# Optimization experiments

Hardware: AMD Instinct MI355X
Metric: run time of the kernel (lower is better)

## Reference

```python
import jax, jax.numpy as jnp
import numpy as np

D = 1024      # query_dim
H = 16        # heads
DH = 64       # dim_head
I = H * DH    # inner_dim = 1024
DC = 768      # context_dim
FF = 4 * D    # ff inner dim = 4096
EPS = 1e-5
SCALE = DH ** -0.5


def setup_inputs() -> dict:
    key = jax.random.key(0)
    ks = jax.random.split(key, 20)
    s = 0.02
    inp = {
        'x': jax.random.normal(ks[0], (2, 2048, D), jnp.float32),
        'context': jax.random.normal(ks[1], (2, 77, DC), jnp.float32),
        'ln1_g': jnp.ones((D,), jnp.float32), 'ln1_b': jnp.zeros((D,), jnp.float32),
        'ln2_g': jnp.ones((D,), jnp.float32), 'ln2_b': jnp.zeros((D,), jnp.float32),
        'ln3_g': jnp.ones((D,), jnp.float32), 'ln3_b': jnp.zeros((D,), jnp.float32),
        'Wq1': jax.random.normal(ks[2], (D, I), jnp.float32) * s,
        'Wk1': jax.random.normal(ks[3], (D, I), jnp.float32) * s,
        'Wv1': jax.random.normal(ks[4], (D, I), jnp.float32) * s,
        'Wo1': jax.random.normal(ks[5], (I, D), jnp.float32) * s,
        'bo1': jnp.zeros((D,), jnp.float32),
        'Wq2': jax.random.normal(ks[6], (D, I), jnp.float32) * s,
        'Wk2': jax.random.normal(ks[7], (DC, I), jnp.float32) * s,
        'Wv2': jax.random.normal(ks[8], (DC, I), jnp.float32) * s,
        'Wo2': jax.random.normal(ks[9], (I, D), jnp.float32) * s,
        'bo2': jnp.zeros((D,), jnp.float32),
        'Wff1': jax.random.normal(ks[10], (D, 2 * FF), jnp.float32) * s,
        'bff1': jnp.zeros((2 * FF,), jnp.float32),
        'Wff2': jax.random.normal(ks[11], (FF, D), jnp.float32) * s,
        'bff2': jnp.zeros((D,), jnp.float32),
    }
    return inp


def layer_norm(x, g, b):
    m = jnp.mean(x, axis=-1, keepdims=True)
    v = jnp.mean(jnp.square(x - m), axis=-1, keepdims=True)
    return (x - m) * jax.lax.rsqrt(v + EPS) * g + b


def cross_attention(x, ctx, Wq, Wk, Wv, Wo, bo):
    # x: [B,N,D], ctx: [B,M,Dc]
    B, N, _ = x.shape
    M = ctx.shape[1]
    q = (x @ Wq).reshape(B, N, H, DH).transpose(0, 2, 1, 3)    # [B,H,N,DH]
    k = (ctx @ Wk).reshape(B, M, H, DH).transpose(0, 2, 1, 3)  # [B,H,M,DH]
    v = (ctx @ Wv).reshape(B, M, H, DH).transpose(0, 2, 1, 3)
    sim = jnp.einsum('bhid,bhjd->bhij', q, k) * SCALE           # [B,H,N,M]
    attn = jax.nn.softmax(sim, axis=-1)
    out = jnp.einsum('bhij,bhjd->bhid', attn, v)                # [B,H,N,DH]
    out = out.transpose(0, 2, 1, 3).reshape(B, N, I)
    return out @ Wo + bo


def reference(x, context, ln1_g, ln1_b, ln2_g, ln2_b, ln3_g, ln3_b,
              Wq1, Wk1, Wv1, Wo1, bo1, Wq2, Wk2, Wv2, Wo2, bo2,
              Wff1, bff1, Wff2, bff2):
    # self-attention
    x = cross_attention(layer_norm(x, ln1_g, ln1_b), layer_norm(x, ln1_g, ln1_b),
                        Wq1, Wk1, Wv1, Wo1, bo1) + x
    # cross-attention
    x = cross_attention(layer_norm(x, ln2_g, ln2_b), context,
                        Wq2, Wk2, Wv2, Wo2, bo2) + x
    # GEGLU feed-forward
    hg = layer_norm(x, ln3_g, ln3_b) @ Wff1 + bff1
    h, gate = hg[..., :FF], hg[..., FF:]
    ff = (h * jax.nn.gelu(gate, approximate=False)) @ Wff2 + bff2
    return ff + x
```

## Files before the change

### kernel.cpp

```cpp
#include <hip/hip_runtime.h>
#include <hip/hip_bf16.h>
#include <math.h>

typedef short short8 __attribute__((ext_vector_type(8)));
typedef float floatx4 __attribute__((ext_vector_type(4)));
typedef unsigned short u16;

#define D_MODEL 1024
#define NH 16
#define DH 64
#define FF_DIM 4096

__device__ __forceinline__ u16 f2b(float f) {
  union { float f; unsigned u; } v; v.f = f;
  unsigned r = (v.u + 0x7fffu + ((v.u >> 16) & 1u)) >> 16;
  return (u16)r;
}
__device__ __forceinline__ u16 f2b_fast(float f) {
  union { float f; unsigned u; } v; v.f = f;
  return (u16)((v.u + 0x8000u) >> 16);
}
__device__ __forceinline__ float b2f(u16 h) {
  union { unsigned u; float f; } v; v.u = ((unsigned)h) << 16;
  return v.f;
}

__device__ __forceinline__ void gl_lds16(const u16* g, u16* l) {
  __builtin_amdgcn_global_load_lds(
      (const __attribute__((address_space(1))) unsigned int*)g,
      (__attribute__((address_space(3))) unsigned int*)l, 16, 0, 0);
}

__launch_bounds__(256)
__global__ void transpose_to_bf16(const float* __restrict__ in, u16* __restrict__ out,
                                  int K, int N, float scale) {
  __shared__ float tile[32][33];
  const int n0 = blockIdx.x * 32;
  const int k0 = blockIdx.y * 32;
  const int tx = threadIdx.x & 31;
  const int ty = threadIdx.x >> 5;
#pragma unroll
  for (int i = 0; i < 4; i++) {
    int k = k0 + ty + i * 8;
    tile[ty + i * 8][tx] = in[(size_t)k * N + (n0 + tx)] * scale;
  }
  __syncthreads();
#pragma unroll
  for (int i = 0; i < 4; i++) {
    int n = n0 + ty + i * 8;
    out[(size_t)n * K + (k0 + tx)] = f2b(tile[tx][ty + i * 8]);
  }
}

__launch_bounds__(256)
__global__ void convert_bf16(const float* __restrict__ in, u16* __restrict__ out, int n) {
  int i = blockIdx.x * 256 + threadIdx.x;
  if (i < n) out[i] = f2b(in[i]);
}

__launch_bounds__(256)
__global__ void ln_to_bf16(const float* __restrict__ x, const float* __restrict__ g,
                           const float* __restrict__ b, u16* __restrict__ out) {
  const int row = blockIdx.x;
  const int tid = threadIdx.x;
  const float4 v = ((const float4*)(x + (size_t)row * D_MODEL))[tid];
  float s = v.x + v.y + v.z + v.w;
  float ss = v.x * v.x + v.y * v.y + v.z * v.z + v.w * v.w;
#pragma unroll
  for (int o = 32; o; o >>= 1) { s += __shfl_xor(s, o); ss += __shfl_xor(ss, o); }
  __shared__ float red[8];
  const int wave = tid >> 6, lane = tid & 63;
  if (lane == 0) { red[wave] = s; red[4 + wave] = ss; }
  __syncthreads();
  const float st = red[0] + red[1] + red[2] + red[3];
  const float sst = red[4] + red[5] + red[6] + red[7];
  const float mean = st * (1.0f / D_MODEL);
  const float var = sst * (1.0f / D_MODEL) - mean * mean;
  const float rs = rsqrtf(var + 1e-5f);
  const float4 gv = ((const float4*)g)[tid];
  const float4 bv = ((const float4*)b)[tid];
  ushort4 o4;
  o4.x = f2b((v.x - mean) * rs * gv.x + bv.x);
  o4.y = f2b((v.y - mean) * rs * gv.y + bv.y);
  o4.z = f2b((v.z - mean) * rs * gv.z + bv.z);
  o4.w = f2b((v.w - mean) * rs * gv.w + bv.w);
  ((ushort4*)(out + (size_t)row * D_MODEL))[tid] = o4;
}

template <int EPI>
__launch_bounds__(256)
__global__ void gemm128(const u16* __restrict__ A, const u16* __restrict__ BT,
                        const float* __restrict__ bias, const float* __restrict__ resid,
                        float* __restrict__ Cf, u16* __restrict__ Cb, u16* __restrict__ VT,
                        int K, int lda, int ldb, int ldc) {
  __shared__ __attribute__((aligned(16))) u16 Al[128 * 32];
  __shared__ __attribute__((aligned(16))) u16 Bl[128 * 32];
  const int tid = threadIdx.x, wave = tid >> 6, lane = tid & 63;
  const int lm = lane & 15, lq = lane >> 4;
  const int wr = (wave >> 1) * 64, wc = (wave & 1) * 64;
  const int m0 = blockIdx.y * 128, n0 = blockIdx.x * 128;

  floatx4 acc[4][4] = {};

  for (int k0 = 0; k0 < K; k0 += 32) {
#pragma unroll
    for (int it = 0; it < 2; it++) {
      const int c = wave * 128 + it * 64 + lane;
      const int r = c >> 2, s = c & 3;
      gl_lds16(A + (size_t)(m0 + r) * lda + k0 + s * 8, &Al[c * 8]);
      gl_lds16(BT + (size_t)(n0 + r) * ldb + k0 + s * 8, &Bl[c * 8]);
    }
    __syncthreads();
    short8 af[4], bf[4];
#pragma unroll
    for (int r = 0; r < 4; r++) af[r] = *(const short8*)(&Al[(wr + r * 16 + lm) * 32 + lq * 8]);
#pragma unroll
    for (int c = 0; c < 4; c++) bf[c] = *(const short8*)(&Bl[(wc + c * 16 + lm) * 32 + lq * 8]);
#pragma unroll
    for (int r = 0; r < 4; r++)
#pragma unroll
      for (int c = 0; c < 4; c++)
        acc[r][c] = __builtin_amdgcn_mfma_f32_16x16x32_bf16(af[r], bf[c], acc[r][c], 0, 0, 0);
    __syncthreads();
  }

#pragma unroll
  for (int r = 0; r < 4; r++)
#pragma unroll
    for (int c = 0; c < 4; c++) {
      const int col = n0 + wc + c * 16 + lm;
      const int row0 = m0 + wr + r * 16 + lq * 4;
      if (EPI == 0) {
#pragma unroll
        for (int i = 0; i < 4; i++)
          Cb[(size_t)(row0 + i) * ldc + col] = f2b(acc[r][c][i]);
      } else if (EPI == 1) {
#pragma unroll
        for (int i = 0; i < 4; i++)
          Cf[(size_t)(row0 + i) * ldc + col] =
              acc[r][c][i] + bias[col] + resid[(size_t)(row0 + i) * ldc + col];
      } else {
        if (col < 2048) {
#pragma unroll
          for (int i = 0; i < 4; i++)
            Cb[(size_t)(row0 + i) * ldc + col] = f2b(acc[r][c][i]);
        } else {
          const int d = col - 2048;
          ushort4 pk;
          pk.x = f2b(acc[r][c][0]); pk.y = f2b(acc[r][c][1]);
          pk.z = f2b(acc[r][c][2]); pk.w = f2b(acc[r][c][3]);
          *(ushort4*)(&VT[((size_t)((row0 >> 11) * 1024 + d)) * 2048 + (row0 & 2047)]) = pk;
        }
      }
    }
}

__launch_bounds__(256)
__global__ void gemm_geglu(const u16* __restrict__ A, const u16* __restrict__ BT,
                           const float* __restrict__ bias, u16* __restrict__ Cb,
                           int K, int lda, int ldb) {
  __shared__ __attribute__((aligned(16))) u16 Al[128 * 32];
  __shared__ __attribute__((aligned(16))) u16 Bl[64 * 32];
  __shared__ __attribute__((aligned(16))) u16 Bg[64 * 32];
  const int tid = threadIdx.x, wave = tid >> 6, lane = tid & 63;
  const int lm = lane & 15, lq = lane >> 4;
  const int wr = (wave >> 1) * 64, wc = (wave & 1) * 32;
  const int m0 = blockIdx.y * 128, n0 = blockIdx.x * 64;

  floatx4 acc[4][2] = {};
  floatx4 accg[4][2] = {};

  for (int k0 = 0; k0 < K; k0 += 32) {
#pragma unroll
    for (int it = 0; it < 2; it++) {
      const int c = wave * 128 + it * 64 + lane;
      const int r = c >> 2, s = c & 3;
      gl_lds16(A + (size_t)(m0 + r) * lda + k0 + s * 8, &Al[c * 8]);
    }
    {
      const int c = wave * 64 + lane;
      const int r = c >> 2, s = c & 3;
      gl_lds16(BT + (size_t)(n0 + r) * ldb + k0 + s * 8, &Bl[c * 8]);
      gl_lds16(BT + (size_t)(n0 + r + FF_DIM) * ldb + k0 + s * 8, &Bg[c * 8]);
    }
    __syncthreads();
    short8 af[4], bf[2], bg[2];
#pragma unroll
    for (int r = 0; r < 4; r++) af[r] = *(const short8*)(&Al[(wr + r * 16 + lm) * 32 + lq * 8]);
#pragma unroll
    for (int c = 0; c < 2; c++) {
      bf[c] = *(const short8*)(&Bl[(wc + c * 16 + lm) * 32 + lq * 8]);
      bg[c] = *(const short8*)(&Bg[(wc + c * 16 + lm) * 32 + lq * 8]);
    }
#pragma unroll
    for (int r = 0; r < 4; r++)
#pragma unroll
      for (int c = 0; c < 2; c++) {
        acc[r][c] = __builtin_amdgcn_mfma_f32_16x16x32_bf16(af[r], bf[c], acc[r][c], 0, 0, 0);
        accg[r][c] = __builtin_amdgcn_mfma_f32_16x16x32_bf16(af[r], bg[c], accg[r][c], 0, 0, 0);
      }
    __syncthreads();
  }

#pragma unroll
  for (int r = 0; r < 4; r++)
#pragma unroll
    for (int c = 0; c < 2; c++) {
      const int col = n0 + wc + c * 16 + lm;
#pragma unroll
      for (int i = 0; i < 4; i++) {
        const int row = m0 + wr + r * 16 + lq * 4 + i;
        const float h = acc[r][c][i] + bias[col];
        const float gt = accg[r][c][i] + bias[col + FF_DIM];
        const float gl = 0.5f * gt * (1.0f + erff(gt * 0.70710678118f));
        Cb[(size_t)row * FF_DIM + col] = f2b(h * gl);
      }
    }
}

#define BM 64
#define BN 64
#define LSTR 40

template <int TRANS>
__launch_bounds__(256)
__global__ void gemm_bt64(const u16* __restrict__ A, const u16* __restrict__ BT,
                          u16* __restrict__ Cb,
                          int M, int N, int K, int lda, int ldb, int ldc, int rowsPerB) {
  __shared__ __attribute__((aligned(16))) u16 Al[BM * LSTR];
  __shared__ __attribute__((aligned(16))) u16 Bl[BN * LSTR];
  const int tid = threadIdx.x, wave = tid >> 6, lane = tid & 63;
  const int wm = (wave >> 1) * 32, wn = (wave & 1) * 32;
  const int lm = lane & 15, lq = lane >> 4;
  const int m0 = blockIdx.y * BM, n0 = blockIdx.x * BN;

  floatx4 acc[2][2] = {};
  const int srow = tid >> 2;
  const int scol = (tid & 3) * 8;
  const bool a_ok = (m0 + srow) < M;

  for (int k0 = 0; k0 < K; k0 += 32) {
    int4 av = make_int4(0, 0, 0, 0);
    if (a_ok) av = *(const int4*)(A + (size_t)(m0 + srow) * lda + k0 + scol);
    *(int4*)(&Al[srow * LSTR + scol]) = av;
    int4 bv = *(const int4*)(BT + (size_t)(n0 + srow) * ldb + k0 + scol);
    *(int4*)(&Bl[srow * LSTR + scol]) = bv;
    __syncthreads();
    short8 af[2], bfr[2];
#pragma unroll
    for (int r = 0; r < 2; r++) af[r] = *(const short8*)(&Al[(wm + r * 16 + lm) * LSTR + lq * 8]);
#pragma unroll
    for (int c = 0; c < 2; c++) bfr[c] = *(const short8*)(&Bl[(wn + c * 16 + lm) * LSTR + lq * 8]);
#pragma unroll
    for (int r = 0; r < 2; r++)
#pragma unroll
      for (int c = 0; c < 2; c++)
        acc[r][c] = __builtin_amdgcn_mfma_f32_16x16x32_bf16(af[r], bfr[c], acc[r][c], 0, 0, 0);
    __syncthreads();
  }

#pragma unroll
  for (int r = 0; r < 2; r++)
#pragma unroll
    for (int c = 0; c < 2; c++) {
      const int col = n0 + wn + c * 16 + lm;
#pragma unroll
      for (int i = 0; i < 4; i++) {
        const int row = m0 + wm + r * 16 + lq * 4 + i;
        if (row < M) {
          if (TRANS == 0) {
            Cb[(size_t)row * ldc + col] = f2b(acc[r][c][i]);
          } else {
            const int bb = row / rowsPerB;
            const int n = row - bb * rowsPerB;
            Cb[((size_t)(bb * 1024 + col)) * 128 + n] = f2b(acc[r][c][i]);
          }
        }
      }
    }
}

__launch_bounds__(256)
__global__ void attn_mfma(const u16* __restrict__ Qg, const u16* __restrict__ Kg,
                          const u16* __restrict__ VTg, u16* __restrict__ Ob,
                          int N, int Mk, int kRowsPerBatch, int ldq, int ldk, int vtld) {
  const int ntiles = N / 64;
  const int bh = blockIdx.x / ntiles;
  const int qt = blockIdx.x % ntiles;
  const int b = bh / NH, h = bh % NH;
  const int tid = threadIdx.x, wave = tid >> 6, lane = tid & 63;
  const int lm = lane & 15, lq = lane >> 4;

  __shared__ __attribute__((aligned(16))) u16 Qs[64 * 64];
  __shared__ __attribute__((aligned(16))) u16 Ks[64 * 64];
  __shared__ __attribute__((aligned(16))) u16 Vt[64 * 64];
  __shared__ __attribute__((aligned(16))) u16 Ps[4][16 * 72];

  const u16* Qh = Qg + (size_t)b * N * ldq + h * DH;
  const u16* Kh = Kg + (size_t)b * kRowsPerBatch * ldk + h * DH;
  const u16* Vh = VTg + (size_t)(b * 1024 + h * DH) * vtld;

  {
    const u16* qsrc = Qh + (size_t)qt * 64 * ldq;
#pragma unroll
    for (int it = 0; it < 2; it++) {
      const int c = wave * 128 + it * 64 + lane;
      const int r = c >> 3, p = c & 7, lc = p ^ (r & 7);
      gl_lds16(qsrc + (size_t)r * ldq + lc * 8, &Qs[c * 8]);
    }
  }
  __syncthreads();
  short8 qf[2];
  qf[0] = *(const short8*)(&Qs[(wave * 16 + lm) * 64 + ((lq) ^ (lm & 7)) * 8]);
  qf[1] = *(const short8*)(&Qs[(wave * 16 + lm) * 64 + ((4 + lq) ^ (lm & 7)) * 8]);

  float lpart[4] = {0.f, 0.f, 0.f, 0.f};
  floatx4 o[4] = {};

  for (int kt = 0; kt < Mk; kt += 64) {
    __syncthreads();
    {
      const u16* ksrc = Kh + (size_t)kt * ldk;
      const u16* vsrc = Vh + kt;
#pragma unroll
      for (int it = 0; it < 2; it++) {
        const int c = wave * 128 + it * 64 + lane;
        const int r = c >> 3, p = c & 7, lc = p ^ (r & 7);
        gl_lds16(ksrc + (size_t)r * ldk + lc * 8, &Ks[c * 8]);
        gl_lds16(vsrc + (size_t)r * vtld + lc * 8, &Vt[c * 8]);
      }
    }
    __syncthreads();

    floatx4 s[4];
#pragma unroll
    for (int ct = 0; ct < 4; ct++) {
      short8 kf0 = *(const short8*)(&Ks[(ct * 16 + lm) * 64 + ((lq) ^ (lm & 7)) * 8]);
      short8 kf1 = *(const short8*)(&Ks[(ct * 16 + lm) * 64 + ((4 + lq) ^ (lm & 7)) * 8]);
      floatx4 z = {};
      z = __builtin_amdgcn_mfma_f32_16x16x32_bf16(qf[0], kf0, z, 0, 0, 0);
      z = __builtin_amdgcn_mfma_f32_16x16x32_bf16(qf[1], kf1, z, 0, 0, 0);
      s[ct] = z;
    }

    if (kt + 64 <= Mk) {
#pragma unroll
      for (int reg = 0; reg < 4; reg++) {
        float p0 = __expf(s[0][reg] - 16.0f);
        float p1 = __expf(s[1][reg] - 16.0f);
        float p2 = __expf(s[2][reg] - 16.0f);
        float p3 = __expf(s[3][reg] - 16.0f);
        lpart[reg] += (p0 + p1) + (p2 + p3);
        const int prow = (lq * 4 + reg) * 72;
        Ps[wave][prow + lm] = f2b_fast(p0);
        Ps[wave][prow + 16 + lm] = f2b_fast(p1);
        Ps[wave][prow + 32 + lm] = f2b_fast(p2);
        Ps[wave][prow + 48 + lm] = f2b_fast(p3);
      }
    } else {
#pragma unroll
      for (int reg = 0; reg < 4; reg++) {
        const int prow = (lq * 4 + reg) * 72;
        float psum = 0.f;
#pragma unroll
        for (int ct = 0; ct < 4; ct++) {
          const bool valid = (kt + ct * 16 + lm) < Mk;
          float p = valid ? __expf(s[ct][reg] - 16.0f) : 0.f;
          psum += p;
          Ps[wave][prow + ct * 16 + lm] = f2b_fast(p);
        }
        lpart[reg] += psum;
      }
    }

    const short8 pf0 = *(const short8*)(&Ps[wave][lm * 72 + lq * 8]);
    const short8 pf1 = *(const short8*)(&Ps[wave][lm * 72 + 32 + lq * 8]);
#pragma unroll
    for (int ct = 0; ct < 4; ct++) {
      short8 vf0 = *(const short8*)(&Vt[(ct * 16 + lm) * 64 + ((lq) ^ (lm & 7)) * 8]);
      short8 vf1 = *(const short8*)(&Vt[(ct * 16 + lm) * 64 + ((4 + lq) ^ (lm & 7)) * 8]);
      o[ct] = __builtin_amdgcn_mfma_f32_16x16x32_bf16(pf0, vf0, o[ct], 0, 0, 0);
      o[ct] = __builtin_amdgcn_mfma_f32_16x16x32_bf16(pf1, vf1, o[ct], 0, 0, 0);
    }
  }

  float inv[4];
#pragma unroll
  for (int reg = 0; reg < 4; reg++) {
    float l = lpart[reg];
    l += __shfl_xor(l, 1); l += __shfl_xor(l, 2);
    l += __shfl_xor(l, 4); l += __shfl_xor(l, 8);
    inv[reg] = 1.0f / l;
  }
#pragma unroll
  for (int ct = 0; ct < 4; ct++)
#pragma unroll
    for (int reg = 0; reg < 4; reg++) {
      const int grow = qt * 64 + wave * 16 + lq * 4 + reg;
      Ob[((size_t)(b * N + grow)) * D_MODEL + h * DH + ct * 16 + lm] =
          f2b(o[ct][reg] * inv[reg]);
    }
}

extern "C" void kernel_launch(void* const* d_in, const int* in_sizes, int n_in,
                              void* d_out, int out_size, void* d_ws, size_t ws_size,
                              hipStream_t stream) {
  const float* x    = (const float*)d_in[0];
  const float* ctx  = (const float*)d_in[1];
  const float* ln1g = (const float*)d_in[2];
  const float* ln1b = (const float*)d_in[3];
  const float* ln2g = (const float*)d_in[4];
  const float* ln2b = (const float*)d_in[5];
  const float* ln3g = (const float*)d_in[6];
  const float* ln3b = (const float*)d_in[7];
  const float* Wq1  = (const float*)d_in[8];
  const float* Wk1  = (const float*)d_in[9];
  const float* Wv1  = (const float*)d_in[10];
  const float* Wo1  = (const float*)d_in[11];
  const float* bo1  = (const float*)d_in[12];
  const float* Wq2  = (const float*)d_in[13];
  const float* Wk2  = (const float*)d_in[14];
  const float* Wv2  = (const float*)d_in[15];
  const float* Wo2  = (const float*)d_in[16];
  const float* bo2  = (const float*)d_in[17];
  const float* Wff1 = (const float*)d_in[18];
  const float* bff1 = (const float*)d_in[19];
  const float* Wff2 = (const float*)d_in[20];
  const float* bff2 = (const float*)d_in[21];
  float* out = (float*)d_out;

  char* ws = (char*)d_ws;
  size_t off = 0;
  auto alloc = [&](size_t bytes) -> char* {
    char* p = ws + off;
    off += (bytes + 255) & ~(size_t)255;
    return p;
  };
  u16* wqkv1T = (u16*)alloc((size_t)3072 * 1024 * 2);
  u16* wo1T   = (u16*)alloc((size_t)1024 * 1024 * 2);
  u16* wq2T   = (u16*)alloc((size_t)1024 * 1024 * 2);
  u16* wk2T   = (u16*)alloc((size_t)1024 * 768 * 2);
  u16* wv2T   = (u16*)alloc((size_t)1024 * 768 * 2);
  u16* wo2T   = (u16*)alloc((size_t)1024 * 1024 * 2);
  u16* wff1T  = (u16*)alloc((size_t)8192 * 1024 * 2);
  u16* wff2T  = (u16*)alloc((size_t)1024 * 4096 * 2);
  u16* xln    = (u16*)alloc((size_t)4096 * 1024 * 2);
  u16* ctxb   = (u16*)alloc((size_t)154 * 768 * 2);
  u16* QKVb   = (u16*)alloc((size_t)4096 * 3072 * 2);
  u16* VTb    = (u16*)alloc((size_t)2048 * 2048 * 2);
  u16* K2b    = (u16*)alloc((size_t)256 * 1024 * 2);
  u16* VT2b   = (u16*)alloc((size_t)2048 * 128 * 2);
  u16* Ob     = (u16*)alloc((size_t)4096 * 1024 * 2);
  float* x1   = (float*)alloc((size_t)4096 * 1024 * 4);
  float* x2   = (float*)alloc((size_t)4096 * 1024 * 4);
  u16* ffin   = (u16*)alloc((size_t)4096 * 4096 * 2);
  u16* Q2b    = ffin;

  dim3 blk(256);

  transpose_to_bf16<<<dim3(32, 32), blk, 0, stream>>>(Wq1, wqkv1T, 1024, 1024, 1.0f);
  transpose_to_bf16<<<dim3(32, 32), blk, 0, stream>>>(Wk1, wqkv1T + (size_t)1024 * 1024, 1024, 1024, 0.125f);
  transpose_to_bf16<<<dim3(32, 32), blk, 0, stream>>>(Wv1, wqkv1T + (size_t)2048 * 1024, 1024, 1024, 1.0f);
  transpose_to_bf16<<<dim3(32, 32), blk, 0, stream>>>(Wo1, wo1T, 1024, 1024, 1.0f);
  transpose_to_bf16<<<dim3(32, 32), blk, 0, stream>>>(Wq2, wq2T, 1024, 1024, 1.0f);
  transpose_to_bf16<<<dim3(32, 24), blk, 0, stream>>>(Wk2, wk2T, 768, 1024, 0.125f);
  transpose_to_bf16<<<dim3(32, 24), blk, 0, stream>>>(Wv2, wv2T, 768, 1024, 1.0f);
  transpose_to_bf16<<<dim3(32, 32), blk, 0, stream>>>(Wo2, wo2T, 1024, 1024, 1.0f);
  transpose_to_bf16<<<dim3(256, 32), blk, 0, stream>>>(Wff1, wff1T, 1024, 8192, 1.0f);
  transpose_to_bf16<<<dim3(32, 128), blk, 0, stream>>>(Wff2, wff2T, 4096, 1024, 1.0f);
  convert_bf16<<<(154 * 768 + 255) / 256, blk, 0, stream>>>(ctx, ctxb, 154 * 768);

  ln_to_bf16<<<4096, blk, 0, stream>>>(x, ln1g, ln1b, xln);
  gemm128<2><<<dim3(24, 32), blk, 0, stream>>>(xln, wqkv1T, nullptr, nullptr, nullptr, QKVb,
                                               VTb, 1024, 1024, 1024, 3072);
  attn_mfma<<<2 * NH * (2048 / 64), blk, 0, stream>>>(QKVb, QKVb + 1024, VTb, Ob,
                                                      2048, 2048, 2048, 3072, 3072, 2048);
  gemm128<1><<<dim3(8, 32), blk, 0, stream>>>(Ob, wo1T, bo1, x, x1, nullptr, nullptr,
                                              1024, 1024, 1024, 1024);

  ln_to_bf16<<<4096, blk, 0, stream>>>(x1, ln2g, ln2b, xln);
  gemm128<0><<<dim3(8, 32), blk, 0, stream>>>(xln, wq2T, nullptr, nullptr, nullptr, Q2b,
                                              nullptr, 1024, 1024, 1024, 1024);
  gemm_bt64<0><<<dim3(16, 3), blk, 0, stream>>>(ctxb, wk2T, K2b, 154, 1024, 768, 768, 768, 1024, 77);
  gemm_bt64<1><<<dim3(16, 3), blk, 0, stream>>>(ctxb, wv2T, VT2b, 154, 1024, 768, 768, 768, 1024, 77);
  attn_mfma<<<2 * NH * (2048 / 64), blk, 0, stream>>>(Q2b, K2b, VT2b, Ob,
                                                      2048, 77, 77, 1024, 1024, 128);
  gemm128<1><<<dim3(8, 32), blk, 0, stream>>>(Ob, wo2T, bo2, x1, x2, nullptr, nullptr,
                                              1024, 1024, 1024, 1024);

  ln_to_bf16<<<4096, blk, 0, stream>>>(x2, ln3g, ln3b, xln);
  gemm_geglu<<<dim3(64, 32), blk, 0, stream>>>(xln, wff1T, bff1, ffin, 1024, 1024, 1024);
  gemm128<1><<<dim3(8, 32), blk, 0, stream>>>(ffin, wff2T, bff2, x2, out, nullptr, nullptr,
                                              4096, 4096, 4096, 1024);
}
```

Measured before the change: 608.6 us.

## Swizzle LDS tiles to avoid bank conflicts and widen GEGLU GEMM tile

Applies an XOR swizzle to the K-chunk placement in shared memory for both gemm128 and gemm_geglu. The global load picks the source column chunk by XOR so that the MFMA fragment reads from LDS land in different banks. Separately, the GEGLU GEMM tile grows from 128x64 to 128x128 per block, doubling the value and gate accumulators and halving the grid, so each loaded A tile is reused across more output columns. This raises register pressure (64 accumulator vectors per thread) and may cut occupancy.

```diff
diff --git a/kernel.cpp b/kernel.cpp
--- a/kernel.cpp
+++ b/kernel.cpp
@@ -99,6 +99,7 @@
   const int lm = lane & 15, lq = lane >> 4;
   const int wr = (wave >> 1) * 64, wc = (wave & 1) * 64;
   const int m0 = blockIdx.y * 128, n0 = blockIdx.x * 128;
+  const int xr = (lm >> 1) & 3;
 
   floatx4 acc[4][4] = {};
 
@@ -107,15 +108,18 @@
     for (int it = 0; it < 2; it++) {
       const int c = wave * 128 + it * 64 + lane;
       const int r = c >> 2, s = c & 3;
-      gl_lds16(A + (size_t)(m0 + r) * lda + k0 + s * 8, &Al[c * 8]);
-      gl_lds16(BT + (size_t)(n0 + r) * ldb + k0 + s * 8, &Bl[c * 8]);
+      const int lc = s ^ ((r >> 1) & 3);
+      gl_lds16(A + (size_t)(m0 + r) * lda + k0 + lc * 8, &Al[c * 8]);
+      gl_lds16(BT + (size_t)(n0 + r) * ldb + k0 + lc * 8, &Bl[c * 8]);
     }
     __syncthreads();
     short8 af[4], bf[4];
 #pragma unroll
-    for (int r = 0; r < 4; r++) af[r] = *(const short8*)(&Al[(wr + r * 16 + lm) * 32 + lq * 8]);
-#pragma unroll
-    for (int c = 0; c < 4; c++) bf[c] = *(const short8*)(&Bl[(wc + c * 16 + lm) * 32 + lq * 8]);
+    for (int r = 0; r < 4; r++)
+      af[r] = *(const short8*)(&Al[(wr + r * 16 + lm) * 32 + (lq ^ xr) * 8]);
+#pragma unroll
+    for (int c = 0; c < 4; c++)
+      bf[c] = *(const short8*)(&Bl[(wc + c * 16 + lm) * 32 + (lq ^ xr) * 8]);
 #pragma unroll
     for (int r = 0; r < 4; r++)
 #pragma unroll
@@ -160,42 +164,41 @@
                            const float* __restrict__ bias, u16* __restrict__ Cb,
                            int K, int lda, int ldb) {
   __shared__ __attribute__((aligned(16))) u16 Al[128 * 32];
-  __shared__ __attribute__((aligned(16))) u16 Bl[64 * 32];
-  __shared__ __attribute__((aligned(16))) u16 Bg[64 * 32];
+  __shared__ __attribute__((aligned(16))) u16 Bl[128 * 32];
+  __shared__ __attribute__((aligned(16))) u16 Bg[128 * 32];
   const int tid = threadIdx.x, wave = tid >> 6, lane = tid & 63;
   const int lm = lane & 15, lq = lane >> 4;
-  const int wr = (wave >> 1) * 64, wc = (wave & 1) * 32;
-  const int m0 = blockIdx.y * 128, n0 = blockIdx.x * 64;
-
-  floatx4 acc[4][2] = {};
-  floatx4 accg[4][2] = {};
+  const int wr = (wave >> 1) * 64, wc = (wave & 1) * 64;
+  const int m0 = blockIdx.y * 128, n0 = blockIdx.x * 128;
+  const int xr = (lm >> 1) & 3;
+
+  floatx4 acc[4][4] = {};
+  floatx4 accg[4][4] = {};
 
   for (int k0 = 0; k0 < K; k0 += 32) {
 #pragma unroll
     for (int it = 0; it < 2; it++) {
       const int c = wave * 128 + it * 64 + lane;
       const int r = c >> 2, s = c & 3;
-      gl_lds16(A + (size_t)(m0 + r) * lda + k0 + s * 8, &Al[c * 8]);
-    }
-    {
-      const int c = wave * 64 + lane;
-      const int r = c >> 2, s = c & 3;
-      gl_lds16(BT + (size_t)(n0 + r) * ldb + k0 + s * 8, &Bl[c * 8]);
-      gl_lds16(BT + (size_t)(n0 + r + FF_DIM) * ldb + k0 + s * 8, &Bg[c * 8]);
-    }
-    __syncthreads();
-    short8 af[4], bf[2], bg[2];
-#pragma unroll
-    for (int r = 0; r < 4; r++) af[r] = *(const short8*)(&Al[(wr + r * 16 + lm) * 32 + lq * 8]);
-#pragma unroll
-    for (int c = 0; c < 2; c++) {
-      bf[c] = *(const short8*)(&Bl[(wc + c * 16 + lm) * 32 + lq * 8]);
-      bg[c] = *(const short8*)(&Bg[(wc + c * 16 + lm) * 32 + lq * 8]);
-    }
+      const int lc = s ^ ((r >> 1) & 3);
+      gl_lds16(A + (size_t)(m0 + r) * lda + k0 + lc * 8, &Al[c * 8]);
+      gl_lds16(BT + (size_t)(n0 + r) * ldb + k0 + lc * 8, &Bl[c * 8]);
+      gl_lds16(BT + (size_t)(n0 + FF_DIM + r) * ldb + k0 + lc * 8, &Bg[c * 8]);
+    }
+    __syncthreads();
+    short8 af[4], bf[4], bg[4];
 #pragma unroll
     for (int r = 0; r < 4; r++)
-#pragma unroll
-      for (int c = 0; c < 2; c++) {
+      af[r] = *(const short8*)(&Al[(wr + r * 16 + lm) * 32 + (lq ^ xr) * 8]);
+#pragma unroll
+    for (int c = 0; c < 4; c++) {
+      bf[c] = *(const short8*)(&Bl[(wc + c * 16 + lm) * 32 + (lq ^ xr) * 8]);
+      bg[c] = *(const short8*)(&Bg[(wc + c * 16 + lm) * 32 + (lq ^ xr) * 8]);
+    }
+#pragma unroll
+    for (int r = 0; r < 4; r++)
+#pragma unroll
+      for (int c = 0; c < 4; c++) {
         acc[r][c] = __builtin_amdgcn_mfma_f32_16x16x32_bf16(af[r], bf[c], acc[r][c], 0, 0, 0);
         accg[r][c] = __builtin_amdgcn_mfma_f32_16x16x32_bf16(af[r], bg[c], accg[r][c], 0, 0, 0);
       }
@@ -205,7 +208,7 @@
 #pragma unroll
   for (int r = 0; r < 4; r++)
 #pragma unroll
-    for (int c = 0; c < 2; c++) {
+    for (int c = 0; c < 4; c++) {
       const int col = n0 + wc + c * 16 + lm;
 #pragma unroll
       for (int i = 0; i < 4; i++) {
@@ -489,7 +492,7 @@
                                               1024, 1024, 1024, 1024);
 
   ln_to_bf16<<<4096, blk, 0, stream>>>(x2, ln3g, ln3b, xln);
-  gemm_geglu<<<dim3(64, 32), blk, 0, stream>>>(xln, wff1T, bff1, ffin, 1024, 1024, 1024);
+  gemm_geglu<<<dim3(32, 32), blk, 0, stream>>>(xln, wff1T, bff1, ffin, 1024, 1024, 1024);
   gemm128<1><<<dim3(8, 32), blk, 0, stream>>>(ffin, wff2T, bff2, x2, out, nullptr, nullptr,
                                               4096, 4096, 4096, 1024);
 }
```

After: 679.9 us. 11.7% more time.
